# Optimization experiments

Measured on AMD Instinct MI355X. Metric: run time of the kernel, lower is better.

Reference implementation:

```python
import jax, jax.numpy as jnp
import numpy as np

EMBED = 256
HEADS = 8
B, T = 8, 1024


def setup_inputs() -> dict:
    key = jax.random.key(0)
    ks = jax.random.split(key, 6)
    scale = 1.0 / np.sqrt(EMBED)
    embeddings = jax.random.normal(ks[0], (B, T, EMBED), dtype=jnp.float32)
    # per-head full-width projections, stacked: [H, out=EMBED, in=EMBED] (torch Linear layout)
    Wq = jax.random.normal(ks[1], (HEADS, EMBED, EMBED), dtype=jnp.float32) * scale
    Wk = jax.random.normal(ks[2], (HEADS, EMBED, EMBED), dtype=jnp.float32) * scale
    Wv = jax.random.normal(ks[3], (HEADS, EMBED, EMBED), dtype=jnp.float32) * scale
    Wo = jax.random.normal(ks[4], (EMBED, HEADS * EMBED), dtype=jnp.float32) * (1.0 / np.sqrt(HEADS * EMBED))
    bo = jax.random.normal(ks[5], (EMBED,), dtype=jnp.float32) * 0.01
    return {"embeddings": embeddings, "Wq": Wq, "Wk": Wk, "Wv": Wv, "Wo": Wo, "bo": bo}


def reference(embeddings, Wq, Wk, Wv, Wo, bo):
    # x: [b,t,e]; W*: [h, out_e, in_e] (torch Linear: y = x @ W.T)
    q = jnp.einsum('bte,hde->hbtd', embeddings, Wq)
    k = jnp.einsum('bte,hde->hbtd', embeddings, Wk)
    v = jnp.einsum('bte,hde->hbtd', embeddings, Wv)
    # NOTE: original code has no 1/sqrt(d) scaling
    energy = jnp.einsum('hbid,hbjd->hbij', q, k)  # [h,b,t,t]
    t = embeddings.shape[1]
    causal = jnp.triu(jnp.ones((t, t), dtype=bool), k=1)
    energy = jnp.where(causal, -jnp.inf, energy)
    attn = jax.nn.softmax(energy, axis=-1)
    o = jnp.einsum('hbij,hbjd->hbid', attn, v)     # [h,b,t,e]
    b, _, _, e = o.shape[1], o.shape[0], o.shape[2], o.shape[3]
    o = jnp.transpose(o, (1, 2, 0, 3)).reshape(embeddings.shape[0], t, -1)  # [b,t,h*e]
    return o @ Wo.T + bo
```

## Files before the change

kernel.cpp:

```cpp
#include <hip/hip_runtime.h>
#include <hip/hip_bf16.h>

#define EMBED 256
#define HEADS 8
#define BATCH 8
#define SEQ   1024
#define NROWS 8192

typedef __attribute__((ext_vector_type(8))) _Float16 half8;
typedef __attribute__((ext_vector_type(4))) float f32x4;
typedef unsigned int  uint;
typedef unsigned short ushort;

#define QE   ((size_t)2097152)

__device__ __forceinline__ ushort f2h(float f) {
    union { _Float16 h; ushort u; } cv; cv.h = (_Float16)f; return cv.u;
}

__global__ __launch_bounds__(256) void convert_f16(
    const float* __restrict__ X,  const float* __restrict__ Wq,
    const float* __restrict__ Wk, const float* __restrict__ Wv,
    const float* __restrict__ Wo,
    ushort* __restrict__ Xf, ushort* __restrict__ Wqkf,
    ushort* __restrict__ Wvf, ushort* __restrict__ Wof)
{
    const int blk = blockIdx.x;
    const float* src; ushort* dst; int i;
    if (blk < 2048)      { src = X;  dst = Xf;            i = blk * 256 + threadIdx.x; }
    else if (blk < 2560) { src = Wq; dst = Wqkf;          i = (blk - 2048) * 256 + threadIdx.x; }
    else if (blk < 3072) { src = Wk; dst = Wqkf + 524288; i = (blk - 2560) * 256 + threadIdx.x; }
    else if (blk < 3584) { src = Wv; dst = Wvf;           i = (blk - 3072) * 256 + threadIdx.x; }
    else                 { src = Wo; dst = Wof;           i = (blk - 3584) * 256 + threadIdx.x; }
    const float4 v = ((const float4*)src)[i];
    uint2 P;
    P.x = (uint)f2h(v.x) | ((uint)f2h(v.y) << 16);
    P.y = (uint)f2h(v.z) | ((uint)f2h(v.w) << 16);
    ((uint2*)dst)[i] = P;
}

__device__ __forceinline__ void gemm1p_core(
    const ushort* __restrict__ Ag, const ushort* __restrict__ Bg,
    ushort* __restrict__ o0, ushort* __restrict__ o1,
    ushort* Ah, ushort* Bh, int m0, int n0, int mode)
{
    const int tid = threadIdx.x, w = tid >> 6, l = tid & 63;
    const int wr = w >> 1, wc = w & 1, g = l >> 4, c16 = l & 15;
    const int sr = l >> 3, sb = l & 7;

    f32x4 acc[4][4];
#pragma unroll
    for (int mi = 0; mi < 4; ++mi)
#pragma unroll
        for (int ni = 0; ni < 4; ++ni) acc[mi][ni] = (f32x4){0.f, 0.f, 0.f, 0.f};

    for (int k0 = 0; k0 < 256; k0 += 64) {
        __syncthreads();
#pragma unroll
        for (int j = 0; j < 4; ++j) {
            const int rb = w * 32 + j * 8;
            const int r  = rb + sr;
            const size_t srcA = (size_t)(m0 + r) * 256 + k0 + ((sb ^ (r & 7)) * 8);
            __builtin_amdgcn_global_load_lds(Ag + srcA, &Ah[rb * 64], 16, 0, 0);
            const size_t srcB = (size_t)(n0 + r) * 256 + k0 + ((sb ^ (r & 7)) * 8);
            __builtin_amdgcn_global_load_lds(Bg + srcB, &Bh[rb * 64], 16, 0, 0);
        }
        asm volatile("s_waitcnt vmcnt(0)" ::: "memory");
        __syncthreads();

#pragma unroll
        for (int kh = 0; kh < 2; ++kh) {
            const int bsel = ((kh << 2) | g) ^ (c16 & 7);
            half8 af[4], bf[4];
#pragma unroll
            for (int mi = 0; mi < 4; ++mi)
                af[mi] = *(const half8*)&Ah[(wr * 64 + mi * 16 + c16) * 64 + bsel * 8];
#pragma unroll
            for (int ni = 0; ni < 4; ++ni)
                bf[ni] = *(const half8*)&Bh[(wc * 64 + ni * 16 + c16) * 64 + bsel * 8];
#pragma unroll
            for (int mi = 0; mi < 4; ++mi)
#pragma unroll
                for (int ni = 0; ni < 4; ++ni)
                    acc[mi][ni] = __builtin_amdgcn_mfma_f32_16x16x32_f16(af[mi], bf[ni], acc[mi][ni], 0, 0, 0);
        }
    }

#pragma unroll
    for (int mi = 0; mi < 4; ++mi)
#pragma unroll
        for (int ni = 0; ni < 4; ++ni) {
            const int n = n0 + wc * 64 + ni * 16 + c16;
            if (mode == 0) {
                const int op = n >> 11, hh = (n >> 8) & 7, d = n & 255;
                ushort* tq = (op ? o1 : o0) + (size_t)hh * QE + d;
#pragma unroll
                for (int j = 0; j < 4; ++j) {
                    const int m = m0 + wr * 64 + mi * 16 + 4 * g + j;
                    tq[(size_t)m * 256] = f2h(acc[mi][ni][j]);
                }
            } else {
#pragma unroll
                for (int j = 0; j < 4; ++j) {
                    const int m = m0 + wr * 64 + mi * 16 + 4 * g + j;
                    o0[(size_t)m * NROWS + n] = f2h(acc[mi][ni][j]);
                }
            }
        }
}

__global__ __launch_bounds__(256) void gemm_qkvt(
    const ushort* __restrict__ Xf,
    const ushort* __restrict__ Wqkf, const ushort* __restrict__ Wvf,
    ushort* __restrict__ qf, ushort* __restrict__ kf, ushort* __restrict__ vtb)
{
    __shared__ __align__(16) ushort Ah[128 * 64];
    __shared__ __align__(16) ushort Bh[128 * 64];
    const int bid = blockIdx.x;
    if (bid < 2048) {
        const int wg = (bid & 7) * 256 + (bid >> 3);
        gemm1p_core(Xf, Wqkf, qf, kf, Ah, Bh, (wg >> 5) * 128, (wg & 31) * 128, 0);
    } else {
        const int b2 = bid - 2048;
        const int wg = (b2 & 7) * 128 + (b2 >> 3);
        gemm1p_core(Wvf, Xf, vtb, nullptr, Ah, Bh, (wg & 15) * 128, (wg >> 4) * 128, 1);
    }
}

__global__ __launch_bounds__(256) void gemm_out_f16(
    const ushort* __restrict__ A, const ushort* __restrict__ Bw,
    const float* __restrict__ bias, float* __restrict__ fo)
{
    __shared__ __align__(16) ushort Ah[64 * 64];
    __shared__ __align__(16) ushort Bh[64 * 64];

    const int wg = (blockIdx.x & 7) * 64 + (blockIdx.x >> 3);
    const int m0 = (wg >> 2) * 64;
    const int n0 = (wg & 3) * 64;

    const int tid = threadIdx.x, w = tid >> 6, l = tid & 63;
    const int wr = w >> 1, wc = w & 1, g = l >> 4, c16 = l & 15;
    const int sr = l >> 3, sb = l & 7;

    f32x4 acc[2][2];
#pragma unroll
    for (int mi = 0; mi < 2; ++mi)
#pragma unroll
        for (int ni = 0; ni < 2; ++ni) acc[mi][ni] = (f32x4){0.f, 0.f, 0.f, 0.f};

    for (int k0 = 0; k0 < 2048; k0 += 64) {
        __syncthreads();
#pragma unroll
        for (int j = 0; j < 2; ++j) {
            const int rb = w * 16 + j * 8;
            const int r  = rb + sr;
            const size_t srcA = (size_t)(m0 + r) * 2048 + k0 + ((sb ^ (r & 7)) * 8);
            __builtin_amdgcn_global_load_lds(A + srcA, &Ah[rb * 64], 16, 0, 0);
            const size_t srcB = (size_t)(n0 + r) * 2048 + k0 + ((sb ^ (r & 7)) * 8);
            __builtin_amdgcn_global_load_lds(Bw + srcB, &Bh[rb * 64], 16, 0, 0);
        }
        asm volatile("s_waitcnt vmcnt(0)" ::: "memory");
        __syncthreads();

#pragma unroll
        for (int kh = 0; kh < 2; ++kh) {
            const int bsel = ((kh << 2) | g) ^ (c16 & 7);
            half8 af[2], bf[2];
#pragma unroll
            for (int mi = 0; mi < 2; ++mi)
                af[mi] = *(const half8*)&Ah[(wr * 32 + mi * 16 + c16) * 64 + bsel * 8];
#pragma unroll
            for (int ni = 0; ni < 2; ++ni)
                bf[ni] = *(const half8*)&Bh[(wc * 32 + ni * 16 + c16) * 64 + bsel * 8];
#pragma unroll
            for (int mi = 0; mi < 2; ++mi)
#pragma unroll
                for (int ni = 0; ni < 2; ++ni)
                    acc[mi][ni] = __builtin_amdgcn_mfma_f32_16x16x32_f16(af[mi], bf[ni], acc[mi][ni], 0, 0, 0);
        }
    }

#pragma unroll
    for (int mi = 0; mi < 2; ++mi)
#pragma unroll
        for (int ni = 0; ni < 2; ++ni) {
            const int n = n0 + wc * 32 + ni * 16 + c16;
            const float bb = bias[n];
#pragma unroll
            for (int j = 0; j < 4; ++j) {
                const int m = m0 + wr * 32 + mi * 16 + 4 * g + j;
                fo[(size_t)m * 256 + n] = acc[mi][ni][j] + bb;
            }
        }
}

__global__ __launch_bounds__(256, 3) void flash_mfma(
    const ushort* __restrict__ qf, const ushort* __restrict__ kf,
    const ushort* __restrict__ vt, ushort* __restrict__ ocf)
{
    __shared__ __align__(16) ushort Ks[2][32 * 256];
    __shared__ __align__(16) ushort VTs[256 * 32];
    __shared__ __align__(16) ushort Pls[4][512];

    const int bid = blockIdx.x;
    const int idx = bid >> 3;
    const int hb  = (bid & 7) * 8 + (idx & 7);
    const int qst = 15 - (idx >> 3);
    const int h = hb >> 3, b = hb & 7;

    const int tid = threadIdx.x;
    const int w = tid >> 6, l = tid & 63;
    const int g = l >> 4, c16 = l & 15;
    const size_t qk_base = (size_t)h * QE + (size_t)b * (SEQ * EMBED);
    const size_t vt_base = (size_t)h * QE + (size_t)b * SEQ;

    const int psw = (c16 >> 1) & 3;
    const int rsw = c16 & 7;
    const int qw0 = qst * 64 + w * 16;
    const int q0 = qw0 + c16;

    half8 qfr[8];
    {
        const ushort* qr = qf + qk_base + (size_t)q0 * EMBED + g * 8;
#pragma unroll
        for (int kc = 0; kc < 8; ++kc)
            qfr[kc] = *(const half8*)(qr + kc * 32);
    }

    const ushort* kbase = kf + qk_base;
    const ushort* vbase = vt + vt_base;
    const int krow_l = l >> 5, kblk = l & 31;
    const int vd_l = l >> 2,  vblk = l & 3;
    uint koff[4], voff[4];
#pragma unroll
    for (int j = 0; j < 4; ++j) {
        const int row = 8 * w + 2 * j + krow_l;
        koff[j] = (uint)(row * EMBED + ((kblk ^ (row & 7)) * 8));
        const int d = w * 64 + j * 16 + vd_l;
        const int phi = ((d >> 1) ^ (d >> 3)) & 3;
        voff[j] = (uint)(d * NROWS + ((vblk ^ phi) * 8));
    }

    f32x4 acc[16];
#pragma unroll
    for (int dt = 0; dt < 16; ++dt) acc[dt] = (f32x4){0.f, 0.f, 0.f, 0.f};
    float m_r = -1e30f, l_p = 0.f;

    char* pw = (char*)&Pls[w][0];
    const int nkt = 2 * qst + 2;

#pragma unroll
    for (int j = 0; j < 4; ++j)
        __builtin_amdgcn_global_load_lds(kbase + koff[j], &Ks[0][(8 * w + 2 * j) * 256], 16, 0, 0);
    asm volatile("s_waitcnt vmcnt(0)" ::: "memory");
    __builtin_amdgcn_s_barrier();
    __builtin_amdgcn_sched_barrier(0);

    for (int kt = 0; kt < nkt; ++kt) {
#pragma unroll
        for (int j = 0; j < 4; ++j)
            __builtin_amdgcn_global_load_lds(vbase + voff[j] + kt * 32,
                                             &VTs[(w * 64 + j * 16) * 32], 16, 0, 0);
        const bool havek = (kt + 1 < nkt);
        if (havek) {
            const ushort* kb = kbase + (size_t)(kt + 1) * (32 * EMBED);
#pragma unroll
            for (int j = 0; j < 4; ++j)
                __builtin_amdgcn_global_load_lds(kb + koff[j],
                                                 &Ks[(kt + 1) & 1][(8 * w + 2 * j) * 256], 16, 0, 0);
        }

        const bool active = (kt * 32 <= qw0 + 15);
        if (active) {
            const ushort* Kb = &Ks[kt & 1][0];
            f32x4 s0 = (f32x4){0.f, 0.f, 0.f, 0.f};
            f32x4 s1 = (f32x4){0.f, 0.f, 0.f, 0.f};
            __builtin_amdgcn_s_setprio(1);
#pragma unroll
            for (int kc = 0; kc < 8; ++kc) {
                const int blk = ((kc * 4 + g) ^ rsw) * 8;
                const half8 a0 = *(const half8*)&Kb[c16 * 256 + blk];
                const half8 a1 = *(const half8*)&Kb[(c16 + 16) * 256 + blk];
                s0 = __builtin_amdgcn_mfma_f32_16x16x32_f16(a0, qfr[kc], s0, 0, 0, 0);
                s1 = __builtin_amdgcn_mfma_f32_16x16x32_f16(a1, qfr[kc], s1, 0, 0, 0);
            }
            __builtin_amdgcn_s_setprio(0);
            const int k0b = kt * 32 + 4 * g;
            float p0[4], p1[4];
            float pm = -1e30f;
#pragma unroll
            for (int r = 0; r < 4; ++r) {
                p0[r] = (k0b + r      > q0) ? -1e30f : s0[r];
                p1[r] = (k0b + 16 + r > q0) ? -1e30f : s1[r];
                pm = fmaxf(pm, fmaxf(p0[r], p1[r]));
            }
            if (__any(pm > m_r + 8.f)) {
                float gm = fmaxf(pm, __shfl_xor(pm, 16));
                gm = fmaxf(gm, __shfl_xor(gm, 32));
                const float mn = fmaxf(m_r, gm);
                const float sc = __expf(m_r - mn);
                l_p *= sc;
#pragma unroll
                for (int dt = 0; dt < 16; ++dt) acc[dt] *= sc;
                m_r = mn;
            }
#pragma unroll
            for (int r = 0; r < 4; ++r) {
                p0[r] = __expf(p0[r] - m_r);
                p1[r] = __expf(p1[r] - m_r);
                l_p += p0[r] + p1[r];
            }
#pragma unroll
            for (int t = 0; t < 2; ++t)
#pragma unroll
                for (int u = 0; u < 2; ++u) {
                    const int kk = 16 * t + 4 * g + 2 * u;
                    const int off = c16 * 64 + (((kk >> 3) ^ psw) * 16) + (kk & 7) * 2;
                    const float lo = t ? p1[2 * u] : p0[2 * u];
                    const float hi = t ? p1[2 * u + 1] : p0[2 * u + 1];
                    *(uint*)(pw + off) = (uint)f2h(lo) | ((uint)f2h(hi) << 16);
                }
        }

        if (havek) asm volatile("s_waitcnt vmcnt(4)" ::: "memory");
        else       asm volatile("s_waitcnt vmcnt(0)" ::: "memory");
        __builtin_amdgcn_s_barrier();
        __builtin_amdgcn_sched_barrier(0);

        if (active) {
            const half8 pfrag = *(const half8*)(pw + c16 * 64 + ((g ^ psw) * 16));
            __builtin_amdgcn_s_setprio(1);
#pragma unroll
            for (int dt = 0; dt < 16; ++dt) {
                const int d = dt * 16 + c16;
                const int phi = ((d >> 1) ^ (d >> 3)) & 3;
                const half8 va = *(const half8*)&VTs[d * 32 + ((g ^ phi) * 8)];
                acc[dt] = __builtin_amdgcn_mfma_f32_16x16x32_f16(va, pfrag, acc[dt], 0, 0, 0);
            }
            __builtin_amdgcn_s_setprio(0);
        }

        asm volatile("s_waitcnt vmcnt(0)" ::: "memory");
        __builtin_amdgcn_s_barrier();
        __builtin_amdgcn_sched_barrier(0);
    }

    l_p += __shfl_xor(l_p, 16);
    l_p += __shfl_xor(l_p, 32);
    const float inv = 1.f / l_p;
    ushort* orow = ocf + ((size_t)(b * SEQ) + q0) * (HEADS * EMBED) + h * EMBED;
#pragma unroll
    for (int dt = 0; dt < 16; ++dt) {
        const f32x4 o = acc[dt] * inv;
        uint2 P2;
        P2.x = (uint)f2h(o[0]) | ((uint)f2h(o[1]) << 16);
        P2.y = (uint)f2h(o[2]) | ((uint)f2h(o[3]) << 16);
        *(uint2*)(orow + dt * 16 + 4 * g) = P2;
    }
}

extern "C" void kernel_launch(void* const* d_in, const int* in_sizes, int n_in,
                              void* d_out, int out_size, void* d_ws, size_t ws_size,
                              hipStream_t stream) {
    const float* X  = (const float*)d_in[0];
    const float* Wq = (const float*)d_in[1];
    const float* Wk = (const float*)d_in[2];
    const float* Wv = (const float*)d_in[3];
    const float* Wo = (const float*)d_in[4];
    const float* bo = (const float*)d_in[5];

    ushort* ws16 = (ushort*)d_ws;
    ushort* qf   = ws16;
    ushort* kf   = ws16 +  8 * QE;
    ushort* vtb  = ws16 + 16 * QE;
    ushort* ocf  = ws16 + 24 * QE;
    ushort* ex   = ws16 + 32 * QE;
    ushort* Xf   = ex;
    ushort* Wqkf = ex + 2097152;
    ushort* Wvf  = ex + 2097152 + 1048576;
    ushort* Wof  = ex + 2097152 + 1048576 + 524288;
    float*  out  = (float*)d_out;

    convert_f16<<<4096, 256, 0, stream>>>(X, Wq, Wk, Wv, Wo, Xf, Wqkf, Wvf, Wof);

    gemm_qkvt<<<3072, 256, 0, stream>>>(Xf, Wqkf, Wvf, qf, kf, vtb);

    flash_mfma<<<1024, 256, 0, stream>>>(qf, kf, vtb, ocf);

    gemm_out_f16<<<512, 256, 0, stream>>>(ocf, Wof, bo, out);
}
```

Baseline: 133.7 us.

## Double-buffer LDS staging in projection and output GEMMs, drop setprio in attention

```diff
diff --git a/kernel.cpp b/kernel.cpp
--- a/kernel.cpp
+++ b/kernel.cpp
@@ -42,7 +42,8 @@
 __device__ __forceinline__ void gemm1p_core(
     const ushort* __restrict__ Ag, const ushort* __restrict__ Bg,
     ushort* __restrict__ o0, ushort* __restrict__ o1,
-    ushort* Ah, ushort* Bh, int m0, int n0, int mode)
+    ushort* Ah, ushort* Bh,
+    int m0, int n0, int mode)
 {
     const int tid = threadIdx.x, w = tid >> 6, l = tid & 63;
     const int wr = w >> 1, wc = w & 1, g = l >> 4, c16 = l & 15;
@@ -54,36 +55,48 @@
 #pragma unroll
         for (int ni = 0; ni < 4; ++ni) acc[mi][ni] = (f32x4){0.f, 0.f, 0.f, 0.f};
 
-    for (int k0 = 0; k0 < 256; k0 += 64) {
-        __syncthreads();
+    auto stage = [&](int buf, int k0) {
 #pragma unroll
         for (int j = 0; j < 4; ++j) {
             const int rb = w * 32 + j * 8;
             const int r  = rb + sr;
             const size_t srcA = (size_t)(m0 + r) * 256 + k0 + ((sb ^ (r & 7)) * 8);
-            __builtin_amdgcn_global_load_lds(Ag + srcA, &Ah[rb * 64], 16, 0, 0);
+            __builtin_amdgcn_global_load_lds(Ag + srcA, &Ah[buf * 8192 + rb * 64], 16, 0, 0);
             const size_t srcB = (size_t)(n0 + r) * 256 + k0 + ((sb ^ (r & 7)) * 8);
-            __builtin_amdgcn_global_load_lds(Bg + srcB, &Bh[rb * 64], 16, 0, 0);
-        }
-        asm volatile("s_waitcnt vmcnt(0)" ::: "memory");
-        __syncthreads();
-
+            __builtin_amdgcn_global_load_lds(Bg + srcB, &Bh[buf * 8192 + rb * 64], 16, 0, 0);
+        }
+    };
+
+    stage(0, 0);
+    asm volatile("s_waitcnt vmcnt(0)" ::: "memory");
+    __builtin_amdgcn_s_barrier();
+    __builtin_amdgcn_sched_barrier(0);
+
+    int cur = 0;
+    for (int t = 0; t < 4; ++t) {
+        if (t < 3) stage(cur ^ 1, (t + 1) * 64);
+        const ushort* Ab = &Ah[cur * 8192];
+        const ushort* Bb = &Bh[cur * 8192];
 #pragma unroll
         for (int kh = 0; kh < 2; ++kh) {
             const int bsel = ((kh << 2) | g) ^ (c16 & 7);
             half8 af[4], bf[4];
 #pragma unroll
             for (int mi = 0; mi < 4; ++mi)
-                af[mi] = *(const half8*)&Ah[(wr * 64 + mi * 16 + c16) * 64 + bsel * 8];
+                af[mi] = *(const half8*)&Ab[(wr * 64 + mi * 16 + c16) * 64 + bsel * 8];
 #pragma unroll
             for (int ni = 0; ni < 4; ++ni)
-                bf[ni] = *(const half8*)&Bh[(wc * 64 + ni * 16 + c16) * 64 + bsel * 8];
+                bf[ni] = *(const half8*)&Bb[(wc * 64 + ni * 16 + c16) * 64 + bsel * 8];
 #pragma unroll
             for (int mi = 0; mi < 4; ++mi)
 #pragma unroll
                 for (int ni = 0; ni < 4; ++ni)
                     acc[mi][ni] = __builtin_amdgcn_mfma_f32_16x16x32_f16(af[mi], bf[ni], acc[mi][ni], 0, 0, 0);
         }
+        asm volatile("s_waitcnt vmcnt(0)" ::: "memory");
+        __builtin_amdgcn_s_barrier();
+        __builtin_amdgcn_sched_barrier(0);
+        cur ^= 1;
     }
 
 #pragma unroll
@@ -114,8 +127,8 @@
     const ushort* __restrict__ Wqkf, const ushort* __restrict__ Wvf,
     ushort* __restrict__ qf, ushort* __restrict__ kf, ushort* __restrict__ vtb)
 {
-    __shared__ __align__(16) ushort Ah[128 * 64];
-    __shared__ __align__(16) ushort Bh[128 * 64];
+    __shared__ __align__(16) ushort Ah[2 * 8192];
+    __shared__ __align__(16) ushort Bh[2 * 8192];
     const int bid = blockIdx.x;
     if (bid < 2048) {
         const int wg = (bid & 7) * 256 + (bid >> 3);
@@ -131,8 +144,8 @@
     const ushort* __restrict__ A, const ushort* __restrict__ Bw,
     const float* __restrict__ bias, float* __restrict__ fo)
 {
-    __shared__ __align__(16) ushort Ah[64 * 64];
-    __shared__ __align__(16) ushort Bh[64 * 64];
+    __shared__ __align__(16) ushort Ah[2 * 4096];
+    __shared__ __align__(16) ushort Bh[2 * 4096];
 
     const int wg = (blockIdx.x & 7) * 64 + (blockIdx.x >> 3);
     const int m0 = (wg >> 2) * 64;
@@ -148,36 +161,48 @@
 #pragma unroll
         for (int ni = 0; ni < 2; ++ni) acc[mi][ni] = (f32x4){0.f, 0.f, 0.f, 0.f};
 
-    for (int k0 = 0; k0 < 2048; k0 += 64) {
-        __syncthreads();
+    auto stage = [&](int buf, int k0) {
 #pragma unroll
         for (int j = 0; j < 2; ++j) {
             const int rb = w * 16 + j * 8;
             const int r  = rb + sr;
             const size_t srcA = (size_t)(m0 + r) * 2048 + k0 + ((sb ^ (r & 7)) * 8);
-            __builtin_amdgcn_global_load_lds(A + srcA, &Ah[rb * 64], 16, 0, 0);
+            __builtin_amdgcn_global_load_lds(A + srcA, &Ah[buf * 4096 + rb * 64], 16, 0, 0);
             const size_t srcB = (size_t)(n0 + r) * 2048 + k0 + ((sb ^ (r & 7)) * 8);
-            __builtin_amdgcn_global_load_lds(Bw + srcB, &Bh[rb * 64], 16, 0, 0);
-        }
-        asm volatile("s_waitcnt vmcnt(0)" ::: "memory");
-        __syncthreads();
-
+            __builtin_amdgcn_global_load_lds(Bw + srcB, &Bh[buf * 4096 + rb * 64], 16, 0, 0);
+        }
+    };
+
+    stage(0, 0);
+    asm volatile("s_waitcnt vmcnt(0)" ::: "memory");
+    __builtin_amdgcn_s_barrier();
+    __builtin_amdgcn_sched_barrier(0);
+
+    int cur = 0;
+    for (int t = 0; t < 32; ++t) {
+        if (t < 31) stage(cur ^ 1, (t + 1) * 64);
+        const ushort* Ab = &Ah[cur * 4096];
+        const ushort* Bb = &Bh[cur * 4096];
 #pragma unroll
         for (int kh = 0; kh < 2; ++kh) {
             const int bsel = ((kh << 2) | g) ^ (c16 & 7);
             half8 af[2], bf[2];
 #pragma unroll
             for (int mi = 0; mi < 2; ++mi)
-                af[mi] = *(const half8*)&Ah[(wr * 32 + mi * 16 + c16) * 64 + bsel * 8];
+                af[mi] = *(const half8*)&Ab[(wr * 32 + mi * 16 + c16) * 64 + bsel * 8];
 #pragma unroll
             for (int ni = 0; ni < 2; ++ni)
-                bf[ni] = *(const half8*)&Bh[(wc * 32 + ni * 16 + c16) * 64 + bsel * 8];
+                bf[ni] = *(const half8*)&Bb[(wc * 32 + ni * 16 + c16) * 64 + bsel * 8];
 #pragma unroll
             for (int mi = 0; mi < 2; ++mi)
 #pragma unroll
                 for (int ni = 0; ni < 2; ++ni)
                     acc[mi][ni] = __builtin_amdgcn_mfma_f32_16x16x32_f16(af[mi], bf[ni], acc[mi][ni], 0, 0, 0);
         }
+        asm volatile("s_waitcnt vmcnt(0)" ::: "memory");
+        __builtin_amdgcn_s_barrier();
+        __builtin_amdgcn_sched_barrier(0);
+        cur ^= 1;
     }
 
 #pragma unroll
@@ -275,7 +300,6 @@
             const ushort* Kb = &Ks[kt & 1][0];
             f32x4 s0 = (f32x4){0.f, 0.f, 0.f, 0.f};
             f32x4 s1 = (f32x4){0.f, 0.f, 0.f, 0.f};
-            __builtin_amdgcn_s_setprio(1);
 #pragma unroll
             for (int kc = 0; kc < 8; ++kc) {
                 const int blk = ((kc * 4 + g) ^ rsw) * 8;
@@ -284,7 +308,6 @@
                 s0 = __builtin_amdgcn_mfma_f32_16x16x32_f16(a0, qfr[kc], s0, 0, 0, 0);
                 s1 = __builtin_amdgcn_mfma_f32_16x16x32_f16(a1, qfr[kc], s1, 0, 0, 0);
             }
-            __builtin_amdgcn_s_setprio(0);
             const int k0b = kt * 32 + 4 * g;
             float p0[4], p1[4];
             float pm = -1e30f;
@@ -329,7 +352,6 @@
 
         if (active) {
             const half8 pfrag = *(const half8*)(pw + c16 * 64 + ((g ^ psw) * 16));
-            __builtin_amdgcn_s_setprio(1);
 #pragma unroll
             for (int dt = 0; dt < 16; ++dt) {
                 const int d = dt * 16 + c16;
@@ -337,7 +359,6 @@
                 const half8 va = *(const half8*)&VTs[d * 32 + ((g ^ phi) * 8)];
                 acc[dt] = __builtin_amdgcn_mfma_f32_16x16x32_f16(va, pfrag, acc[dt], 0, 0, 0);
             }
-            __builtin_amdgcn_s_setprio(0);
         }
 
         asm volatile("s_waitcnt vmcnt(0)" ::: "memory");
```

New measurement: 136.7 us. 1.02x slower.

## Load V fragments directly from global into registers, drop V LDS staging

Applied to the files above, without the earlier changes.

```diff
diff --git a/kernel.cpp b/kernel.cpp
--- a/kernel.cpp
+++ b/kernel.cpp
@@ -199,7 +199,6 @@
     const ushort* __restrict__ vt, ushort* __restrict__ ocf)
 {
     __shared__ __align__(16) ushort Ks[2][32 * 256];
-    __shared__ __align__(16) ushort VTs[256 * 32];
     __shared__ __align__(16) ushort Pls[4][512];
 
     const int bid = blockIdx.x;
@@ -228,17 +227,14 @@
     }
 
     const ushort* kbase = kf + qk_base;
-    const ushort* vbase = vt + vt_base;
+    const ushort* vbl = vt + vt_base + (size_t)c16 * NROWS + g * 8;
+
     const int krow_l = l >> 5, kblk = l & 31;
-    const int vd_l = l >> 2,  vblk = l & 3;
-    uint koff[4], voff[4];
+    uint koff[4];
 #pragma unroll
     for (int j = 0; j < 4; ++j) {
         const int row = 8 * w + 2 * j + krow_l;
         koff[j] = (uint)(row * EMBED + ((kblk ^ (row & 7)) * 8));
-        const int d = w * 64 + j * 16 + vd_l;
-        const int phi = ((d >> 1) ^ (d >> 3)) & 3;
-        voff[j] = (uint)(d * NROWS + ((vblk ^ phi) * 8));
     }
 
     f32x4 acc[16];
@@ -257,10 +253,6 @@
     __builtin_amdgcn_sched_barrier(0);
 
     for (int kt = 0; kt < nkt; ++kt) {
-#pragma unroll
-        for (int j = 0; j < 4; ++j)
-            __builtin_amdgcn_global_load_lds(vbase + voff[j] + kt * 32,
-                                             &VTs[(w * 64 + j * 16) * 32], 16, 0, 0);
         const bool havek = (kt + 1 < nkt);
         if (havek) {
             const ushort* kb = kbase + (size_t)(kt + 1) * (32 * EMBED);
@@ -272,10 +264,15 @@
 
         const bool active = (kt * 32 <= qw0 + 15);
         if (active) {
+            const ushort* vkt = vbl + kt * 32;
+            half8 vfA0 = *(const half8*)(vkt + (size_t)0 * (16 * NROWS));
+            half8 vfA1 = *(const half8*)(vkt + (size_t)1 * (16 * NROWS));
+            half8 vfA2 = *(const half8*)(vkt + (size_t)2 * (16 * NROWS));
+            half8 vfA3 = *(const half8*)(vkt + (size_t)3 * (16 * NROWS));
+
             const ushort* Kb = &Ks[kt & 1][0];
             f32x4 s0 = (f32x4){0.f, 0.f, 0.f, 0.f};
             f32x4 s1 = (f32x4){0.f, 0.f, 0.f, 0.f};
-            __builtin_amdgcn_s_setprio(1);
 #pragma unroll
             for (int kc = 0; kc < 8; ++kc) {
                 const int blk = ((kc * 4 + g) ^ rsw) * 8;
@@ -284,7 +281,6 @@
                 s0 = __builtin_amdgcn_mfma_f32_16x16x32_f16(a0, qfr[kc], s0, 0, 0, 0);
                 s1 = __builtin_amdgcn_mfma_f32_16x16x32_f16(a1, qfr[kc], s1, 0, 0, 0);
             }
-            __builtin_amdgcn_s_setprio(0);
             const int k0b = kt * 32 + 4 * g;
             float p0[4], p1[4];
             float pm = -1e30f;
@@ -320,24 +316,39 @@
                     const float hi = t ? p1[2 * u + 1] : p0[2 * u + 1];
                     *(uint*)(pw + off) = (uint)f2h(lo) | ((uint)f2h(hi) << 16);
                 }
-        }
-
-        if (havek) asm volatile("s_waitcnt vmcnt(4)" ::: "memory");
-        else       asm volatile("s_waitcnt vmcnt(0)" ::: "memory");
-        __builtin_amdgcn_s_barrier();
-        __builtin_amdgcn_sched_barrier(0);
-
-        if (active) {
             const half8 pfrag = *(const half8*)(pw + c16 * 64 + ((g ^ psw) * 16));
-            __builtin_amdgcn_s_setprio(1);
-#pragma unroll
-            for (int dt = 0; dt < 16; ++dt) {
-                const int d = dt * 16 + c16;
-                const int phi = ((d >> 1) ^ (d >> 3)) & 3;
-                const half8 va = *(const half8*)&VTs[d * 32 + ((g ^ phi) * 8)];
-                acc[dt] = __builtin_amdgcn_mfma_f32_16x16x32_f16(va, pfrag, acc[dt], 0, 0, 0);
-            }
-            __builtin_amdgcn_s_setprio(0);
+
+            half8 vfB0 = *(const half8*)(vkt + (size_t)4 * (16 * NROWS));
+            half8 vfB1 = *(const half8*)(vkt + (size_t)5 * (16 * NROWS));
+            half8 vfB2 = *(const half8*)(vkt + (size_t)6 * (16 * NROWS));
+            half8 vfB3 = *(const half8*)(vkt + (size_t)7 * (16 * NROWS));
+            acc[0] = __builtin_amdgcn_mfma_f32_16x16x32_f16(vfA0, pfrag, acc[0], 0, 0, 0);
+            acc[1] = __builtin_amdgcn_mfma_f32_16x16x32_f16(vfA1, pfrag, acc[1], 0, 0, 0);
+            acc[2] = __builtin_amdgcn_mfma_f32_16x16x32_f16(vfA2, pfrag, acc[2], 0, 0, 0);
+            acc[3] = __builtin_amdgcn_mfma_f32_16x16x32_f16(vfA3, pfrag, acc[3], 0, 0, 0);
+
+            vfA0 = *(const half8*)(vkt + (size_t)8  * (16 * NROWS));
+            vfA1 = *(const half8*)(vkt + (size_t)9  * (16 * NROWS));
+            vfA2 = *(const half8*)(vkt + (size_t)10 * (16 * NROWS));
+            vfA3 = *(const half8*)(vkt + (size_t)11 * (16 * NROWS));
+            acc[4] = __builtin_amdgcn_mfma_f32_16x16x32_f16(vfB0, pfrag, acc[4], 0, 0, 0);
+            acc[5] = __builtin_amdgcn_mfma_f32_16x16x32_f16(vfB1, pfrag, acc[5], 0, 0, 0);
+            acc[6] = __builtin_amdgcn_mfma_f32_16x16x32_f16(vfB2, pfrag, acc[6], 0, 0, 0);
+            acc[7] = __builtin_amdgcn_mfma_f32_16x16x32_f16(vfB3, pfrag, acc[7], 0, 0, 0);
+
+            vfB0 = *(const half8*)(vkt + (size_t)12 * (16 * NROWS));
+            vfB1 = *(const half8*)(vkt + (size_t)13 * (16 * NROWS));
+            vfB2 = *(const half8*)(vkt + (size_t)14 * (16 * NROWS));
+            vfB3 = *(const half8*)(vkt + (size_t)15 * (16 * NROWS));
+            acc[8]  = __builtin_amdgcn_mfma_f32_16x16x32_f16(vfA0, pfrag, acc[8],  0, 0, 0);
+            acc[9]  = __builtin_amdgcn_mfma_f32_16x16x32_f16(vfA1, pfrag, acc[9],  0, 0, 0);
+            acc[10] = __builtin_amdgcn_mfma_f32_16x16x32_f16(vfA2, pfrag, acc[10], 0, 0, 0);
+            acc[11] = __builtin_amdgcn_mfma_f32_16x16x32_f16(vfA3, pfrag, acc[11], 0, 0, 0);
+
+            acc[12] = __builtin_amdgcn_mfma_f32_16x16x32_f16(vfB0, pfrag, acc[12], 0, 0, 0);
+            acc[13] = __builtin_amdgcn_mfma_f32_16x16x32_f16(vfB1, pfrag, acc[13], 0, 0, 0);
+            acc[14] = __builtin_amdgcn_mfma_f32_16x16x32_f16(vfB2, pfrag, acc[14], 0, 0, 0);
+            acc[15] = __builtin_amdgcn_mfma_f32_16x16x32_f16(vfB3, pfrag, acc[15], 0, 0, 0);
         }
 
         asm volatile("s_waitcnt vmcnt(0)" ::: "memory");
```

Result: slower. 216.8 us (+62.1%).
